# Optimization experiments

Measured on AMD Instinct MI355X. Metric: run time of the kernel, lower is better.

Reference implementation:

```python
import jax, jax.numpy as jnp
from jax import lax
import numpy as np

B, T, S, Q = 256, 128, 16, 16
E, K = 128, 20
VOCAB = 50000 + K  # vocab_size + num_blocks (key slots appended)


def prelu(x, a):
    return jnp.where(x > 0, x, a * x)


def setup_inputs() -> dict:
    key = jax.random.key(0)
    ks = jax.random.split(key, 12)
    story = jax.random.randint(ks[0], (B, T, S), 0, 50000, dtype=jnp.int64 if jax.config.jax_enable_x64 else jnp.int32)
    query = jax.random.randint(ks[1], (B, Q), 0, 50000, dtype=jnp.int64 if jax.config.jax_enable_x64 else jnp.int32)
    embed_table = jax.random.normal(ks[2], (VOCAB, E), jnp.float32) * 0.1
    embed_table = embed_table.at[0].set(0.0)  # padding_idx=0
    story_mask = jnp.ones((S, E), jnp.float32)
    query_mask = jnp.ones((Q, E), jnp.float32)
    prelu_a = jnp.ones((E,), jnp.float32)
    U = jax.random.normal(ks[3], (E, E), jnp.float32) * 0.1
    V = jax.random.normal(ks[4], (E, E), jnp.float32) * 0.1
    W = jax.random.normal(ks[5], (E, E), jnp.float32) * 0.1
    bias = jax.random.normal(ks[6], (E,), jnp.float32) * 0.1
    H = jax.random.normal(ks[7], (E, E), jnp.float32) * 0.1
    R = jax.random.normal(ks[8], (VOCAB, E), jnp.float32) * 0.1
    return {"story": story, "query": query, "embed_table": embed_table,
            "story_mask": story_mask, "query_mask": query_mask, "prelu_a": prelu_a,
            "U": U, "V": V, "W": W, "bias": bias, "H": H, "R": R}


def reference(story, query, embed_table, story_mask, query_mask, prelu_a, U, V, W, bias, H, R):
    # encode story: (B,T,S,E) * (S,E) summed over S -> (B,T,E)
    s_enc = jnp.sum(embed_table[story] * story_mask, axis=2)
    # encode query: (B,Q,E) * (Q,E) summed over Q -> (B,E)
    q_enc = jnp.sum(embed_table[query] * query_mask, axis=1)

    keys = embed_table[VOCAB - K:]              # (K,E) block keys
    state0 = jnp.broadcast_to(keys[None], (B, K, E))
    key_V = keys @ V.T                           # (K,E), loop-invariant

    def step(state, x):                          # state (B,K,E), x (B,E)
        gate = jax.nn.sigmoid(jnp.einsum('be,bke->bk', x, state) + x @ keys.T)  # (B,K)
        cand = prelu(jnp.einsum('bke,fe->bkf', state, U) + bias
                     + (x @ W.T)[:, None, :] + key_V[None], prelu_a)
        ns = state + gate[..., None] * cand
        norm = jnp.linalg.norm(ns, axis=-1, keepdims=True) + 1e-8
        ns = jnp.where(ns > 0, ns, 1.0) / norm   # Threshold(0,1) then L2-normalize
        return ns, None

    state, _ = lax.scan(step, state0, jnp.swapaxes(s_enc, 0, 1))  # scan over T

    # output module
    att = jax.nn.softmax(jnp.einsum('bke,be->bk', state, q_enc), axis=-1)
    u = jnp.einsum('bk,bke->be', att, state)
    y = prelu(q_enc + u @ H.T, prelu_a) @ R.T    # (B,VOCAB)
    return y
```

## Files before the change

kernel.cpp:

```cpp
#include <hip/hip_runtime.h>
#include <hip/hip_bf16.h>
#include <stdint.h>

#define BB 256
#define TT 128
#define SS 16
#define QQ 16
#define EE 128
#define KK 20
#define VOCAB 50020
#define KB_ROWS 10
#define XK_STR 24

typedef __attribute__((ext_vector_type(8))) _Float16 h8v;
typedef __attribute__((ext_vector_type(2))) __fp16 fp2v;
typedef __attribute__((ext_vector_type(4))) unsigned short u4h;
typedef __attribute__((ext_vector_type(4))) float f4v;
#define MFMA16(a,b,c) __builtin_amdgcn_mfma_f32_16x16x32_f16(a,b,c,0,0,0)

static __device__ __forceinline__ unsigned pk2u(fp2v h){
  union { fp2v h; unsigned u; } c; c.h = h; return c.u;
}
static __device__ __forceinline__ float pk_lo(fp2v h){ return (float)h[0]; }
static __device__ __forceinline__ float pk_hi(fp2v h){ return (float)h[1]; }
static __device__ __forceinline__ unsigned short h1u(_Float16 h){
  union { _Float16 h; unsigned short u; } c; c.h = h; return c.u;
}
static __device__ __forceinline__ void split2_8(const float* v, h8v& h, h8v& l){
  #pragma unroll
  for (int j=0;j<8;++j){
    _Float16 hb = (_Float16)v[j];
    float hf = (float)hb;
    h[j] = hb;
    l[j] = (_Float16)(v[j]-hf);
  }
}
static __device__ __forceinline__ float dpp_add16(float x){
  int v;
  v = __builtin_amdgcn_update_dpp(0, __float_as_int(x), 0xB1, 0xF, 0xF, true);
  x += __int_as_float(v);
  v = __builtin_amdgcn_update_dpp(0, __float_as_int(x), 0x4E, 0xF, 0xF, true);
  x += __int_as_float(v);
  v = __builtin_amdgcn_update_dpp(0, __float_as_int(x), 0x124, 0xF, 0xF, true);
  x += __int_as_float(v);
  v = __builtin_amdgcn_update_dpp(0, __float_as_int(x), 0x128, 0xF, 0xF, true);
  x += __int_as_float(v);
  return x;
}
template<int IMM>
static __device__ __forceinline__ u4h tr_read(unsigned va){
  u4h d;
  asm volatile("ds_read_b64_tr_b16 %0, %1 offset:%c2" : "=v"(d) : "v"(va), "i"(IMM));
  return d;
}
static __device__ __forceinline__ h8v cat8h(u4h a, u4h b){
  union { u4h p[2]; h8v v; } u; u.p[0]=a; u.p[1]=b; return u.v;
}
#define LDA(P,K4) cat8h(tr_read<(P)*4096+(K4)*1024>(va), tr_read<(P)*4096+(K4)*1024+128>(va))

static const size_t OFF_SENC = 0;
static const size_t OFF_QENC = OFF_SENC + (size_t)BB*TT*EE;
static const size_t OFF_CKF  = OFF_QENC + (size_t)BB*EE;
static const size_t OFF_XW   = OFF_CKF  + (size_t)KK*EE;
static const size_t OFF_Z    = OFF_XW   + (size_t)BB*TT*EE;
static const size_t OFF_XK   = OFF_Z    + (size_t)BB*EE;
static const size_t OFF_ST   = OFF_XK   + (size_t)BB*TT*XK_STR;

__global__ __launch_bounds__(256) void k_embed_sum(
    const int* __restrict__ tok, const float* __restrict__ emb,
    const float* __restrict__ mask, float* __restrict__ out,
    int nrow)
{
  int tid = threadIdx.x;
  int row = blockIdx.x*8 + (tid>>5);
  if (row >= nrow) return;
  int e4 = (tid&31)*4;
  float4 acc = make_float4(0.f,0.f,0.f,0.f);
  #pragma unroll
  for (int s=0; s<16; ++s) {
    int id = tok[row*16 + s];
    float4 ev = *(const float4*)(emb + (size_t)id*EE + e4);
    float4 mv = *(const float4*)(mask + s*EE + e4);
    acc.x += ev.x*mv.x; acc.y += ev.y*mv.y; acc.z += ev.z*mv.z; acc.w += ev.w*mv.w;
  }
  *(float4*)(out + (size_t)row*EE + e4) = acc;
}

__global__ __launch_bounds__(128) void k_ckf(
    const float* __restrict__ emb, const float* __restrict__ V,
    const float* __restrict__ bias, float* __restrict__ Ckf)
{
  int k = blockIdx.x;
  int f = threadIdx.x;
  const float* key = emb + (size_t)(VOCAB-KK+k)*EE;
  const float* vr  = V + (size_t)f*EE;
  float acc = bias[f];
  for (int e=0; e<EE; e+=4) {
    float4 kv = *(const float4*)(key + e);
    float4 vv = *(const float4*)(vr + e);
    acc += kv.x*vv.x + kv.y*vv.y + kv.z*vv.z + kv.w*vv.w;
  }
  Ckf[k*EE + f] = acc;
}

__global__ __launch_bounds__(256) void k_xw(
    const float* __restrict__ senc, const float* __restrict__ W,
    const float* __restrict__ emb, float* __restrict__ xw,
    float* __restrict__ xk)
{
  __shared__ float xs[64*EE];
  __shared__ float keys_s[KK*EE];
  int tid = threadIdx.x;
  int r0 = blockIdx.x*64;
  for (int i=0;i<8;++i){
    int idx = tid + i*256; int r = idx>>5; int c4 = (idx&31)*4;
    *(float4*)(xs + r*EE + c4) = *(const float4*)(senc + (size_t)(r0+r)*EE + c4);
  }
  for (int idx=tid; idx<KK*EE; idx+=256)
    keys_s[idx] = emb[(size_t)(VOCAB-KK + (idx>>7))*EE + (idx&127)];
  __syncthreads();
  int f  = tid & 127;
  int rh = tid >> 7;
  float acc[32];
  #pragma unroll
  for (int i=0;i<32;++i) acc[i]=0.f;
  const float* wr = W + (size_t)f*EE;
  for (int e4=0; e4<EE; e4+=4) {
    float4 w4 = *(const float4*)(wr + e4);
    #pragma unroll
    for (int rr=0; rr<32; ++rr) {
      float4 x4 = *(const float4*)(xs + (rh*32+rr)*EE + e4);
      acc[rr] += w4.x*x4.x + w4.y*x4.y + w4.z*x4.z + w4.w*x4.w;
    }
  }
  #pragma unroll
  for (int rr=0; rr<32; ++rr)
    xw[(size_t)(r0 + rh*32 + rr)*EE + f] = acc[rr];
  for (int i=0;i<5;++i){
    int task = tid + i*256;
    int r = task/KK, k = task - r*KK;
    float a = 0.f;
    for (int e=0; e<EE; e+=4){
      float4 x4 = *(const float4*)(xs + r*EE + e);
      float4 k4 = *(const float4*)(keys_s + k*EE + e);
      a += x4.x*k4.x + x4.y*k4.y + x4.z*k4.z + x4.w*k4.w;
    }
    int ki = k < 10 ? k : k + 2;
    xk[(size_t)(r0+r)*XK_STR + ki] = a;
  }
}

struct ScanLds {
  unsigned short st[2][2][EE][16];
  unsigned short xp[2][2][EE];
  float npart[2][4][16];
};

__global__ __launch_bounds__(256) void k_scan(
    const float* __restrict__ emb, const float* __restrict__ U,
    const float* __restrict__ senc, const float* __restrict__ xw,
    const float* __restrict__ xk, const float* __restrict__ Ckf,
    const float* __restrict__ prelu_a, float* __restrict__ zst)
{
  __shared__ ScanLds L;
  int tid = threadIdx.x;
  int bid = blockIdx.x;
  int b   = bid >> 1, kb = bid & 1;
  int l   = tid & 63, cg = tid >> 6;
  int q   = l >> 4,  c  = l & 15;
  int col[2] = { cg*32 + c, cg*32 + 16 + c };

  for (int idx = tid; idx < 2*2*EE*16; idx += 256) ((unsigned short*)L.st)[idx] = 0;
  __syncthreads();
  for (int idx = tid; idx < KB_ROWS*EE; idx += 256){
    int row = idx >> 7, e = idx & 127;
    float v = emb[(size_t)(VOCAB - KK + kb*KB_ROWS + row)*EE + e];
    _Float16 hb = (_Float16)v;
    _Float16 lb = (_Float16)(v - (float)hb);
    L.st[0][0][e][row] = h1u(hb);
    L.st[0][1][e][row] = h1u(lb);
  }
  h8v bh[2][4], bl[2][4];
  #pragma unroll
  for (int nt=0;nt<2;++nt)
    #pragma unroll
    for (int kk=0;kk<4;++kk){
      float tmp[8];
      const float* up = U + (size_t)col[nt]*EE + kk*32 + q*8;
      *(float4*)&tmp[0] = *(const float4*)up;
      *(float4*)&tmp[4] = *(const float4*)(up+4);
      split2_8(tmp, bh[nt][kk], bl[nt][kk]);
    }
  float Creg[2][4], pa2[2], nsv[2][4];
  bool realr[4];
  #pragma unroll
  for (int r=0;r<4;++r) realr[r] = (4*q + r) < KB_ROWS;
  #pragma unroll
  for (int nt=0;nt<2;++nt){
    pa2[nt] = prelu_a[col[nt]];
    #pragma unroll
    for (int r=0;r<4;++r){
      int lr = 4*q + r;
      Creg[nt][r] = realr[r] ? Ckf[(kb*KB_ROWS+lr)*EE + col[nt]] : 0.f;
      nsv[nt][r]  = realr[r] ? emb[(size_t)(VOCAB-KK+kb*KB_ROWS+lr)*EE + col[nt]] : 0.f;
    }
  }

  const float* xrow  = senc + (size_t)b*TT*EE;
  const float* xwrow = xw   + (size_t)b*TT*EE;
  const float* xkrow = xk   + (size_t)b*TT*XK_STR + kb*12;

  if (tid < EE){
    float v = xrow[tid];
    _Float16 hb = (_Float16)v;
    _Float16 lb = (_Float16)(v - (float)hb);
    L.xp[0][0][tid] = h1u(hb); L.xp[0][1][tid] = h1u(lb);
  }
  float xwc[2] = { xwrow[col[0]], xwrow[col[1]] };
  float xkc[4];
  {
    f4v xk4 = {0.f,0.f,0.f,0.f};
    if (q < 3) xk4 = *(const f4v*)(xkrow + 4*q);
    #pragma unroll
    for (int r=0;r<4;++r) xkc[r] = realr[r] ? xk4[r] : 0.f;
  }

  unsigned va0 = (unsigned)(uintptr_t)&L.st[0][0][0][0] + q*256 + c*8;
  __syncthreads();

  for (int t=0; t<TT; ++t){
    int p = t & 1, pn = p ^ 1;
    unsigned va = va0 + p*8192;
    const unsigned short (*xpp)[EE] = L.xp[p];

    float invr[4];
    if (t > 0){
      f4v p0 = *(const f4v*)&L.npart[p][0][4*q];
      f4v p1 = *(const f4v*)&L.npart[p][1][4*q];
      f4v p2 = *(const f4v*)&L.npart[p][2][4*q];
      f4v p3 = *(const f4v*)&L.npart[p][3][4*q];
      f4v ss = p0 + p1 + p2 + p3;
      #pragma unroll
      for (int r=0;r<4;++r)
        invr[r] = __builtin_amdgcn_rcpf(__builtin_amdgcn_sqrtf(ss[r]) + 1e-8f);
    } else {
      #pragma unroll
      for (int r=0;r<4;++r) invr[r] = 1.0f;
    }

    float nxv = 0.f, xwn[2] = {0.f,0.f};
    f4v xk4n = {0.f,0.f,0.f,0.f};
    if (t+1 < TT){
      if (tid < EE) nxv = xrow[(size_t)(t+1)*EE + tid];
      xwn[0] = xwrow[(size_t)(t+1)*EE + col[0]];
      xwn[1] = xwrow[(size_t)(t+1)*EE + col[1]];
      if (q < 3) xk4n = *(const f4v*)(xkrow + (size_t)(t+1)*XK_STR + 4*q);
    }

    h8v Ah[4] = { LDA(0,0), LDA(0,1), LDA(0,2), LDA(0,3) };
    h8v Al[4] = { LDA(1,0), LDA(1,1), LDA(1,2), LDA(1,3) };
    asm volatile("s_waitcnt lgkmcnt(0)" ::: "memory");
    __builtin_amdgcn_sched_barrier(0);

    f4v z4 = {0.f,0.f,0.f,0.f};
    f4v acc[2][2] = {{z4,z4},{z4,z4}};
    f4v gac[2] = {z4,z4};
    #pragma unroll
    for (int kk=0; kk<4; ++kk){
      int h = kk>>1;
      h8v xh = *(const h8v*)&xpp[0][kk*32 + q*8];
      h8v xl = *(const h8v*)&xpp[1][kk*32 + q*8];
      #pragma unroll
      for (int nt=0;nt<2;++nt){
        acc[nt][h] = MFMA16(Al[kk], bh[nt][kk], acc[nt][h]);
        acc[nt][h] = MFMA16(Ah[kk], bl[nt][kk], acc[nt][h]);
        acc[nt][h] = MFMA16(Ah[kk], bh[nt][kk], acc[nt][h]);
      }
      gac[h] = MFMA16(Al[kk], xh, gac[h]);
      gac[h] = MFMA16(Ah[kk], xl, gac[h]);
      gac[h] = MFMA16(Ah[kk], xh, gac[h]);
    }
    f4v acc0 = acc[0][0] + acc[0][1];
    f4v acc1 = acc[1][0] + acc[1][1];
    f4v gacc = gac[0] + gac[1];

    float s2[4];
    #pragma unroll
    for (int r=0;r<4;++r){
      float graw = gacc[r]*invr[r] + xkc[r];
      float g = __builtin_amdgcn_rcpf(1.0f + __builtin_amdgcn_exp2f(-1.442695040889f * graw));
      float s2r = 0.f;
      #pragma unroll
      for (int nt=0;nt<2;++nt){
        float so = nsv[nt][r] * invr[r];
        float cv = (nt ? acc1[r] : acc0[r])*invr[r] + Creg[nt][r] + xwc[nt];
        cv = cv > 0.f ? cv : pa2[nt]*cv;
        float n = so + g*cv;
        nsv[nt][r] = realr[r] ? (n > 0.f ? n : 1.0f) : 0.f;
        s2r += n*n;
      }
      s2[r] = dpp_add16(s2r);
    }
    if (c == 0){
      f4v np; np[0]=s2[0]; np[1]=s2[1]; np[2]=s2[2]; np[3]=s2[3];
      *(f4v*)&L.npart[pn][cg][4*q] = np;
    }

    #pragma unroll
    for (int nt=0;nt<2;++nt){
      float v0=nsv[nt][0], v1=nsv[nt][1], v2=nsv[nt][2], v3=nsv[nt][3];
      fp2v pa = __builtin_amdgcn_cvt_pkrtz(v0, v1);
      fp2v pb = __builtin_amdgcn_cvt_pkrtz(v2, v3);
      float r0 = v0 - pk_lo(pa);
      float r1 = v1 - pk_hi(pa);
      float r2 = v2 - pk_lo(pb);
      float r3 = v3 - pk_hi(pb);
      fp2v pc = __builtin_amdgcn_cvt_pkrtz(r0, r1);
      fp2v pd = __builtin_amdgcn_cvt_pkrtz(r2, r3);
      *(uint2*)&L.st[pn][0][col[nt]][4*q] = make_uint2(pk2u(pa), pk2u(pb));
      *(uint2*)&L.st[pn][1][col[nt]][4*q] = make_uint2(pk2u(pc), pk2u(pd));
    }
    if (t+1 < TT && tid < EE){
      _Float16 hb = (_Float16)nxv;
      _Float16 lb = (_Float16)(nxv - (float)hb);
      L.xp[pn][0][tid] = h1u(hb); L.xp[pn][1][tid] = h1u(lb);
    }
    xwc[0]=xwn[0]; xwc[1]=xwn[1];
    #pragma unroll
    for (int r=0;r<4;++r) xkc[r] = realr[r] ? xk4n[r] : 0.f;
    __syncthreads();
  }

  {
    int pf = TT & 1;
    f4v p0 = *(const f4v*)&L.npart[pf][0][4*q];
    f4v p1 = *(const f4v*)&L.npart[pf][1][4*q];
    f4v p2 = *(const f4v*)&L.npart[pf][2][4*q];
    f4v p3 = *(const f4v*)&L.npart[pf][3][4*q];
    f4v ss = p0 + p1 + p2 + p3;
    #pragma unroll
    for (int r=0;r<4;++r){
      if (realr[r]){
        float inv = __builtin_amdgcn_rcpf(__builtin_amdgcn_sqrtf(ss[r]) + 1e-8f);
        #pragma unroll
        for (int nt=0;nt<2;++nt)
          zst[((size_t)b*KK + kb*KB_ROWS + 4*q + r)*EE + col[nt]] = nsv[nt][r]*inv;
      }
    }
  }
}

__global__ __launch_bounds__(128) void k_tail(
    const float* __restrict__ zst, const float* __restrict__ qenc,
    const float* __restrict__ prelu_a, const float* __restrict__ H,
    float* __restrict__ zout)
{
  __shared__ float st[KK*EE];
  __shared__ float us[EE];
  __shared__ float red[2][KK];
  __shared__ float gs[KK];
  int b = blockIdx.x, tid = threadIdx.x;
  for (int i = tid; i < KK*EE; i += 128) st[i] = zst[(size_t)b*KK*EE + i];
  float qv = qenc[(size_t)b*EE + tid];
  __syncthreads();
  int wv = tid >> 6, ln = tid & 63;
  for (int k=0;k<KK;++k){
    float p = qv * st[k*EE + tid];
    #pragma unroll
    for (int off=32; off; off>>=1) p += __shfl_xor(p, off);
    if (ln == 0) red[wv][k] = p;
  }
  __syncthreads();
  if (tid == 0){
    float mx = -1e30f, gg[KK];
    for (int k=0;k<KK;++k){ float v = red[0][k]+red[1][k]; gg[k]=v; mx = fmaxf(mx, v); }
    float s = 0.f;
    for (int k=0;k<KK;++k){ float e_ = expf(gg[k]-mx); gg[k]=e_; s += e_; }
    for (int k=0;k<KK;++k) gs[k] = gg[k]/s;
  }
  __syncthreads();
  float u_ = 0.f;
  #pragma unroll
  for (int k=0;k<KK;++k) u_ += gs[k]*st[k*EE + tid];
  us[tid] = u_;
  __syncthreads();
  float hp = 0.f;
  const float* hr = H + (size_t)tid*EE;
  for (int e=0; e<EE; e+=4){
    float4 h4 = *(const float4*)(hr + e);
    float4 u4 = *(const float4*)(us + e);
    hp += h4.x*u4.x + h4.y*u4.y + h4.z*u4.z + h4.w*u4.w;
  }
  float zv = qv + hp;
  float pat = prelu_a[tid];
  zv = zv > 0.f ? zv : pat*zv;
  zout[(size_t)b*EE + tid] = zv;
}

__global__ __launch_bounds__(256) void k_out(
    const float* __restrict__ z, const float* __restrict__ R,
    float* __restrict__ y)
{
  int tid = threadIdx.x;
  int w = tid >> 6, l = tid & 63;
  int q = l >> 4, cc = l & 15;
  int b0 = blockIdx.y * 32;
  int vbase = blockIdx.x * 256 + w * 64;

  h8v ah[2][4], al[2][4];
  #pragma unroll
  for (int mt=0;mt<2;++mt){
    const float* zr = z + (size_t)(b0 + mt*16 + cc)*EE;
    #pragma unroll
    for (int kk=0;kk<4;++kk){
      float tmp[8];
      *(float4*)&tmp[0] = *(const float4*)(zr + kk*32 + q*8);
      *(float4*)&tmp[4] = *(const float4*)(zr + kk*32 + q*8 + 4);
      split2_8(tmp, ah[mt][kk], al[mt][kk]);
    }
  }
  #pragma unroll
  for (int vt=0; vt<4; ++vt){
    int v = vbase + vt*16 + cc;
    int vc = v < VOCAB ? v : VOCAB-1;
    const float* rr = R + (size_t)vc*EE;
    h8v bh[4], bl[4];
    #pragma unroll
    for (int kk=0;kk<4;++kk){
      float tmp[8];
      *(float4*)&tmp[0] = *(const float4*)(rr + kk*32 + q*8);
      *(float4*)&tmp[4] = *(const float4*)(rr + kk*32 + q*8 + 4);
      split2_8(tmp, bh[kk], bl[kk]);
    }
    f4v acc0 = {0.f,0.f,0.f,0.f};
    f4v acc1 = {0.f,0.f,0.f,0.f};
    #pragma unroll
    for (int kk=0;kk<4;++kk){
      acc0 = MFMA16(al[0][kk], bh[kk], acc0);
      acc0 = MFMA16(ah[0][kk], bl[kk], acc0);
      acc0 = MFMA16(ah[0][kk], bh[kk], acc0);
      acc1 = MFMA16(al[1][kk], bh[kk], acc1);
      acc1 = MFMA16(ah[1][kk], bl[kk], acc1);
      acc1 = MFMA16(ah[1][kk], bh[kk], acc1);
    }
    if (v < VOCAB){
      #pragma unroll
      for (int r=0;r<4;++r){
        y[(size_t)(b0 + q*4 + r)*VOCAB + v]      = acc0[r];
        y[(size_t)(b0 + 16 + q*4 + r)*VOCAB + v] = acc1[r];
      }
    }
  }
}

extern "C" void kernel_launch(void* const* d_in, const int* in_sizes, int n_in,
                              void* d_out, int out_size, void* d_ws, size_t ws_size,
                              hipStream_t stream)
{
  const int*   story = (const int*)d_in[0];
  const int*   query = (const int*)d_in[1];
  const float* emb   = (const float*)d_in[2];
  const float* smask = (const float*)d_in[3];
  const float* qmask = (const float*)d_in[4];
  const float* pa    = (const float*)d_in[5];
  const float* U     = (const float*)d_in[6];
  const float* V     = (const float*)d_in[7];
  const float* W     = (const float*)d_in[8];
  const float* bias  = (const float*)d_in[9];
  const float* H     = (const float*)d_in[10];
  const float* R     = (const float*)d_in[11];
  float* y  = (float*)d_out;
  float* ws = (float*)d_ws;

  float* s_enc = ws + OFF_SENC;
  float* q_enc = ws + OFF_QENC;
  float* Ckf   = ws + OFF_CKF;
  float* xw    = ws + OFF_XW;
  float* z     = ws + OFF_Z;
  float* xk    = ws + OFF_XK;
  float* zst   = ws + OFF_ST;

  k_embed_sum<<<dim3(BB*TT/8), 256, 0, stream>>>(story, emb, smask, s_enc, BB*TT);
  k_embed_sum<<<dim3(BB/8),    256, 0, stream>>>(query, emb, qmask, q_enc, BB);
  k_ckf<<<dim3(KK), 128, 0, stream>>>(emb, V, bias, Ckf);
  k_xw<<<dim3(BB*TT/64), 256, 0, stream>>>(s_enc, W, emb, xw, xk);

  k_scan<<<dim3(BB*2), 256, 0, stream>>>(emb, U, s_enc, xw, xk, Ckf, pa, zst);
  k_tail<<<dim3(BB), 128, 0, stream>>>(zst, q_enc, pa, H, z);

  k_out<<<dim3((VOCAB+255)/256, BB/32), 256, 0, stream>>>(z, R, y);
}
```

Measured before the change: 379.1 us.

## Fuse story embedding into xw kernel, merge small kernels, widen output batch tile

Story embedding sums are now computed inside the xw projection kernel, which writes them directly to shared memory and to s_enc. This removes a separate launch and the re-read of s_enc. The query embedding and key/V projection are merged into one small kernel, cutting the launch count from seven to five. The output GEMM now covers 64 batch rows per block instead of 32, halving reads of the large R matrix at the cost of more registers per thread, which may lower occupancy.

Result: slower. 390.8 us (+3.1%).

```diff
diff --git a/kernel.cpp b/kernel.cpp
--- a/kernel.cpp
+++ b/kernel.cpp
@@ -66,46 +66,47 @@
 static const size_t OFF_XK   = OFF_Z    + (size_t)BB*EE;
 static const size_t OFF_ST   = OFF_XK   + (size_t)BB*TT*XK_STR;
 
-__global__ __launch_bounds__(256) void k_embed_sum(
-    const int* __restrict__ tok, const float* __restrict__ emb,
-    const float* __restrict__ mask, float* __restrict__ out,
-    int nrow)
+__global__ __launch_bounds__(256) void k_small(
+    const int* __restrict__ query, const float* __restrict__ emb,
+    const float* __restrict__ qmask, const float* __restrict__ V,
+    const float* __restrict__ bias, float* __restrict__ qenc,
+    float* __restrict__ Ckf)
 {
   int tid = threadIdx.x;
-  int row = blockIdx.x*8 + (tid>>5);
-  if (row >= nrow) return;
-  int e4 = (tid&31)*4;
-  float4 acc = make_float4(0.f,0.f,0.f,0.f);
-  #pragma unroll
-  for (int s=0; s<16; ++s) {
-    int id = tok[row*16 + s];
-    float4 ev = *(const float4*)(emb + (size_t)id*EE + e4);
-    float4 mv = *(const float4*)(mask + s*EE + e4);
-    acc.x += ev.x*mv.x; acc.y += ev.y*mv.y; acc.z += ev.z*mv.z; acc.w += ev.w*mv.w;
-  }
-  *(float4*)(out + (size_t)row*EE + e4) = acc;
-}
-
-__global__ __launch_bounds__(128) void k_ckf(
-    const float* __restrict__ emb, const float* __restrict__ V,
-    const float* __restrict__ bias, float* __restrict__ Ckf)
-{
-  int k = blockIdx.x;
-  int f = threadIdx.x;
-  const float* key = emb + (size_t)(VOCAB-KK+k)*EE;
-  const float* vr  = V + (size_t)f*EE;
-  float acc = bias[f];
-  for (int e=0; e<EE; e+=4) {
-    float4 kv = *(const float4*)(key + e);
-    float4 vv = *(const float4*)(vr + e);
-    acc += kv.x*vv.x + kv.y*vv.y + kv.z*vv.z + kv.w*vv.w;
-  }
-  Ckf[k*EE + f] = acc;
-}
-
-__global__ __launch_bounds__(256) void k_xw(
-    const float* __restrict__ senc, const float* __restrict__ W,
-    const float* __restrict__ emb, float* __restrict__ xw,
+  int bid = blockIdx.x;
+  if (bid < BB/8){
+    int row = bid*8 + (tid>>5);
+    int e4 = (tid&31)*4;
+    float4 acc = make_float4(0.f,0.f,0.f,0.f);
+    #pragma unroll
+    for (int s=0; s<QQ; ++s) {
+      int id = query[row*QQ + s];
+      float4 ev = *(const float4*)(emb + (size_t)id*EE + e4);
+      float4 mv = *(const float4*)(qmask + s*EE + e4);
+      acc.x += ev.x*mv.x; acc.y += ev.y*mv.y; acc.z += ev.z*mv.z; acc.w += ev.w*mv.w;
+    }
+    *(float4*)(qenc + (size_t)row*EE + e4) = acc;
+  } else {
+    int k = bid - BB/8;
+    if (tid < 128){
+      int f = tid;
+      const float* key = emb + (size_t)(VOCAB-KK+k)*EE;
+      const float* vr  = V + (size_t)f*EE;
+      float acc = bias[f];
+      for (int e=0; e<EE; e+=4) {
+        float4 kv = *(const float4*)(key + e);
+        float4 vv = *(const float4*)(vr + e);
+        acc += kv.x*vv.x + kv.y*vv.y + kv.z*vv.z + kv.w*vv.w;
+      }
+      Ckf[k*EE + f] = acc;
+    }
+  }
+}
+
+__global__ __launch_bounds__(256) void k_enc_xw(
+    const int* __restrict__ tok, const float* __restrict__ emb,
+    const float* __restrict__ smask, const float* __restrict__ W,
+    float* __restrict__ senc, float* __restrict__ xw,
     float* __restrict__ xk)
 {
   __shared__ float xs[64*EE];
@@ -113,8 +114,18 @@
   int tid = threadIdx.x;
   int r0 = blockIdx.x*64;
   for (int i=0;i<8;++i){
-    int idx = tid + i*256; int r = idx>>5; int c4 = (idx&31)*4;
-    *(float4*)(xs + r*EE + c4) = *(const float4*)(senc + (size_t)(r0+r)*EE + c4);
+    int row = i*8 + (tid>>5);
+    int e4 = (tid&31)*4;
+    float4 acc = make_float4(0.f,0.f,0.f,0.f);
+    #pragma unroll
+    for (int s=0; s<SS; ++s) {
+      int id = tok[(size_t)(r0+row)*SS + s];
+      float4 ev = *(const float4*)(emb + (size_t)id*EE + e4);
+      float4 mv = *(const float4*)(smask + s*EE + e4);
+      acc.x += ev.x*mv.x; acc.y += ev.y*mv.y; acc.z += ev.z*mv.z; acc.w += ev.w*mv.w;
+    }
+    *(float4*)(xs + row*EE + e4) = acc;
+    *(float4*)(senc + (size_t)(r0+row)*EE + e4) = acc;
   }
   for (int idx=tid; idx<KK*EE; idx+=256)
     keys_s[idx] = emb[(size_t)(VOCAB-KK + (idx>>7))*EE + (idx&127)];
@@ -404,12 +415,12 @@
   int tid = threadIdx.x;
   int w = tid >> 6, l = tid & 63;
   int q = l >> 4, cc = l & 15;
-  int b0 = blockIdx.y * 32;
+  int b0 = blockIdx.y * 64;
   int vbase = blockIdx.x * 256 + w * 64;
 
-  h8v ah[2][4], al[2][4];
-  #pragma unroll
-  for (int mt=0;mt<2;++mt){
+  h8v ah[4][4], al[4][4];
+  #pragma unroll
+  for (int mt=0;mt<4;++mt){
     const float* zr = z + (size_t)(b0 + mt*16 + cc)*EE;
     #pragma unroll
     for (int kk=0;kk<4;++kk){
@@ -434,6 +445,8 @@
     }
     f4v acc0 = {0.f,0.f,0.f,0.f};
     f4v acc1 = {0.f,0.f,0.f,0.f};
+    f4v acc2 = {0.f,0.f,0.f,0.f};
+    f4v acc3 = {0.f,0.f,0.f,0.f};
     #pragma unroll
     for (int kk=0;kk<4;++kk){
       acc0 = MFMA16(al[0][kk], bh[kk], acc0);
@@ -442,12 +455,20 @@
       acc1 = MFMA16(al[1][kk], bh[kk], acc1);
       acc1 = MFMA16(ah[1][kk], bl[kk], acc1);
       acc1 = MFMA16(ah[1][kk], bh[kk], acc1);
+      acc2 = MFMA16(al[2][kk], bh[kk], acc2);
+      acc2 = MFMA16(ah[2][kk], bl[kk], acc2);
+      acc2 = MFMA16(ah[2][kk], bh[kk], acc2);
+      acc3 = MFMA16(al[3][kk], bh[kk], acc3);
+      acc3 = MFMA16(ah[3][kk], bl[kk], acc3);
+      acc3 = MFMA16(ah[3][kk], bh[kk], acc3);
     }
     if (v < VOCAB){
       #pragma unroll
       for (int r=0;r<4;++r){
-        y[(size_t)(b0 + q*4 + r)*VOCAB + v]      = acc0[r];
+        y[(size_t)(b0 +      q*4 + r)*VOCAB + v] = acc0[r];
         y[(size_t)(b0 + 16 + q*4 + r)*VOCAB + v] = acc1[r];
+        y[(size_t)(b0 + 32 + q*4 + r)*VOCAB + v] = acc2[r];
+        y[(size_t)(b0 + 48 + q*4 + r)*VOCAB + v] = acc3[r];
       }
     }
   }
@@ -480,13 +501,11 @@
   float* xk    = ws + OFF_XK;
   float* zst   = ws + OFF_ST;
 
-  k_embed_sum<<<dim3(BB*TT/8), 256, 0, stream>>>(story, emb, smask, s_enc, BB*TT);
-  k_embed_sum<<<dim3(BB/8),    256, 0, stream>>>(query, emb, qmask, q_enc, BB);
-  k_ckf<<<dim3(KK), 128, 0, stream>>>(emb, V, bias, Ckf);
-  k_xw<<<dim3(BB*TT/64), 256, 0, stream>>>(s_enc, W, emb, xw, xk);
+  k_small<<<dim3(BB/8 + KK), 256, 0, stream>>>(query, emb, qmask, V, bias, q_enc, Ckf);
+  k_enc_xw<<<dim3(BB*TT/64), 256, 0, stream>>>(story, emb, smask, W, s_enc, xw, xk);
 
   k_scan<<<dim3(BB*2), 256, 0, stream>>>(emb, U, s_enc, xw, xk, Ckf, pa, zst);
   k_tail<<<dim3(BB), 128, 0, stream>>>(zst, q_enc, pa, H, z);
 
-  k_out<<<dim3((VOCAB+255)/256, BB/32), 256, 0, stream>>>(z, R, y);
-}
+  k_out<<<dim3((VOCAB+255)/256, BB/64), 256, 0, stream>>>(z, R, y);
+}
```
